# Kernel optimization log

Hardware: AMD Instinct MI355X
Metric: run time of the kernel (lower is better)

The kernel has to match this reference:

```python
import jax, jax.numpy as jnp
import numpy as np
import math

B, S, D = 2, 1024, 1024
H = 16
HD = D // H
E = 8
DFF = 4096
EPS = 1e-5


def _ln(x, g, b):
    m = jnp.mean(x, axis=-1, keepdims=True)
    v = jnp.mean((x - m) ** 2, axis=-1, keepdims=True)
    return (x - m) / jnp.sqrt(v + EPS) * g + b


def setup_inputs() -> dict:
    key = jax.random.key(0)
    ks = jax.random.split(key, 16)
    s = 0.02
    inp = {
        'src': jax.random.normal(ks[0], (B, S, D), jnp.float32),
        'qw': jax.random.normal(ks[1], (D, D), jnp.float32) * s,
        'kw': jax.random.normal(ks[2], (D, D), jnp.float32) * s,
        'vw': jax.random.normal(ks[3], (D, D), jnp.float32) * s,
        'ow': jax.random.normal(ks[4], (D, D), jnp.float32) * s,
        'gate_w': jax.random.normal(ks[5], (D, D), jnp.float32) * s,
        'gate_b': jax.random.normal(ks[6], (D,), jnp.float32) * s,
        'scale_w': jax.random.normal(ks[7], (H, HD), jnp.float32) * s,
        'n1_g': jnp.ones((D,), jnp.float32),
        'n1_b': jnp.zeros((D,), jnp.float32),
        'n2_g': jnp.ones((D,), jnp.float32),
        'n2_b': jnp.zeros((D,), jnp.float32),
        'moe_gate_w': jax.random.normal(ks[8], (D, E), jnp.float32) * s,
        'moe_gate_b': jnp.zeros((E,), jnp.float32),
        'w1': jax.random.normal(ks[9], (E, D, DFF), jnp.float32) * s,
        'b1': jnp.zeros((E, DFF), jnp.float32),
        'ln_g': jnp.ones((E, DFF), jnp.float32),
        'ln_b': jnp.zeros((E, DFF), jnp.float32),
        'w2': jax.random.normal(ks[10], (E, DFF, D), jnp.float32) * s,
        'b2': jnp.zeros((E, D), jnp.float32),
        'res_scale': jnp.ones((E,), jnp.float32),
    }
    return inp


def _forward(src, qw, kw, vw, ow, gate_w, gate_b, scale_w, n1_g, n1_b, n2_g, n2_b,
             moe_gate_w, moe_gate_b, w1, b1, ln_g, ln_b, w2, b2, res_scale):
    # ---- MemoAttention (non-flash path, eval: no dropout, no mask) ----
    q = (src @ qw).reshape(B, S, H, HD).transpose(0, 2, 1, 3)  # [B,H,S,HD]
    k = (src @ kw).reshape(B, S, H, HD).transpose(0, 2, 1, 3)
    v = (src @ vw).reshape(B, S, H, HD).transpose(0, 2, 1, 3)
    scores = jnp.einsum('bhqd,bhkd->bhqk', q, k) / math.sqrt(HD)
    # dynamic per-(head,query) scale gate
    scale = jax.nn.sigmoid(jnp.einsum('bhsd,hd->bhs', q, scale_w)) * 2.0
    scores = scores * scale[..., None]
    attn = jax.nn.softmax(scores, axis=-1)
    out = jnp.einsum('bhqk,bhkd->bhqd', attn, v)
    out = out.transpose(0, 2, 1, 3).reshape(B, S, D)
    gate = jax.nn.sigmoid(out @ gate_w + gate_b)
    attn_out = (out * gate) @ ow

    x = _ln(src + attn_out, n1_g, n1_b)

    # ---- MoE FFN (top-2 routing; eval: no gate noise; capacity never exceeded) ----
    xf = x.reshape(-1, D)                      # [T, D]
    T = xf.shape[0]
    logits = xf @ moe_gate_w + moe_gate_b      # [T, E]
    top_v, top_i = jax.lax.top_k(logits, 2)
    # NB: original sums BOTH top-k softmax weights per token (== 1.0), and the
    wsum = jnp.sum(jax.nn.softmax(top_v, axis=-1), axis=-1)   # [T] (== 1)
    e_sel = jnp.max(top_i, axis=-1)                           # [T]
    # dense per-expert FFN on all tokens, then per-token select (masked compute)
    h = jnp.einsum('td,edf->etf', xf, w1) + b1[:, None, :]    # [E,T,DFF]
    h = _ln(h, ln_g[:, None, :], ln_b[:, None, :])
    h = jax.nn.gelu(h, approximate=False)                     # torch nn.GELU (erf)
    y = jnp.einsum('etf,efd->etd', h, w2) + b2[:, None, :]    # [E,T,D]
    y = y * res_scale[:, None, None] + xf[None]
    sel = jnp.take_along_axis(y, e_sel[None, :, None], axis=0)[0]  # [T,D]
    moe_out = (sel * wsum[:, None]).reshape(B, S, D)

    return _ln(x + moe_out, n2_g, n2_b)


def reference(src, qw, kw, vw, ow, gate_w, gate_b, scale_w, n1_g, n1_b, n2_g, n2_b,
              moe_gate_w, moe_gate_b, w1, b1, ln_g, ln_b, w2, b2, res_scale):
    return _forward(src, qw, kw, vw, ow, gate_w, gate_b, scale_w, n1_g, n1_b,
                    n2_g, n2_b, moe_gate_w, moe_gate_b, w1, b1, ln_g, ln_b,
                    w2, b2, res_scale)
```

## Files before the change

kernel.cpp:

```cpp
#include <hip/hip_runtime.h>
#include <math.h>

#define TOK    2048
#define DMODEL 1024
#define NHEAD  16
#define HDIM   64
#define NEXP   8
#define DFFN   4096

typedef unsigned short u16;
typedef __attribute__((ext_vector_type(8))) short short8;
typedef __attribute__((ext_vector_type(4))) float floatx4;

__device__ __forceinline__ float sigmoidf_(float x) { return 1.f / (1.f + __expf(-x)); }

__device__ __forceinline__ u16 f2bf(float f) {
  union { float f; unsigned u; } v; v.f = f;
  unsigned r = v.u + 0x7FFFu + ((v.u >> 16) & 1u);
  return (u16)(r >> 16);
}
__device__ __forceinline__ float bf2f(u16 h) {
  union { unsigned u; float f; } v; v.u = ((unsigned)h) << 16; return v.f;
}

__device__ __forceinline__ void gload16(const void* g, void* l) {
  __builtin_amdgcn_global_load_lds((const __attribute__((address_space(1))) void*)g,
                                   (__attribute__((address_space(3))) void*)l, 16, 0, 0);
}

__device__ __forceinline__ float blockReduceSum256(float val) {
  __shared__ float ws_[4];
  #pragma unroll
  for (int off = 32; off; off >>= 1) val += __shfl_down(val, off);
  int lane = threadIdx.x & 63, w = threadIdx.x >> 6;
  if (lane == 0) ws_[w] = val;
  __syncthreads();
  float r = ws_[0] + ws_[1] + ws_[2] + ws_[3];
  __syncthreads();
  return r;
}

__global__ __launch_bounds__(256) void prep_kernel(
    const float* __restrict__ src, u16* __restrict__ Shi, u16* __restrict__ Slo,
    const float* __restrict__ Qw, const float* __restrict__ Kw, const float* __restrict__ Vw,
    u16* __restrict__ W3h, u16* __restrict__ W3l,
    const float* __restrict__ Gw, u16* __restrict__ Gh, u16* __restrict__ Gl,
    const float* __restrict__ Ow, u16* __restrict__ Oh, u16* __restrict__ Ol) {
  const int bid = blockIdx.x, tid = threadIdx.x;
  __shared__ float tile[32][33];
  if (bid < 2048) {
    const int i = bid * 256 + tid;
    const float4 v = ((const float4*)src)[i];
    const float f[4] = {v.x, v.y, v.z, v.w};
    union { u16 s[4]; uint2 u; } h, l;
    #pragma unroll
    for (int j = 0; j < 4; ++j) {
      h.s[j] = f2bf(f[j]);
      l.s[j] = f2bf(f[j] - bf2f(h.s[j]));
    }
    ((uint2*)Shi)[i] = h.u;
    ((uint2*)Slo)[i] = l.u;
    return;
  }
  const float* W; u16 *Whp, *Wlp; int n0, k0, ldk;
  if (bid < 5120) {
    const int t = bid - 2048;
    const int z = t >> 5;
    const int zz = z >> 5;
    W = (zz == 0) ? Qw : (zz == 1) ? Kw : Vw;
    Whp = W3h + (size_t)zz * DMODEL * DMODEL;
    Wlp = W3l + (size_t)zz * DMODEL * DMODEL;
    n0 = (t & 31) * 32; k0 = (z & 31) * 32; ldk = DMODEL;
  } else {
    const int t = bid - 5120;
    const int t2 = t & 1023;
    if (t < 1024) { W = Gw; Whp = Gh; Wlp = Gl; }
    else          { W = Ow; Whp = Oh; Wlp = Ol; }
    n0 = (t2 & 31) * 32; k0 = (t2 >> 5) * 32; ldk = DMODEL;
  }
  const int r = tid >> 3, c4 = (tid & 7) * 4;
  const float4 v = *(const float4*)&W[(size_t)(k0 + r) * DMODEL + n0 + c4];
  tile[r][c4+0] = v.x; tile[r][c4+1] = v.y; tile[r][c4+2] = v.z; tile[r][c4+3] = v.w;
  __syncthreads();
  union { u16 s[4]; uint2 u; } h, l;
  #pragma unroll
  for (int j = 0; j < 4; ++j) {
    const float f = tile[c4 + j][r];
    h.s[j] = f2bf(f);
    l.s[j] = f2bf(f - bf2f(h.s[j]));
  }
  *(uint2*)&Whp[(size_t)(n0 + r) * ldk + k0 + c4] = h.u;
  *(uint2*)&Wlp[(size_t)(n0 + r) * ldk + k0 + c4] = l.u;
}

template<int EPI, int TN>
__device__ __forceinline__ void gemm_split_body(
    u16* Ah, u16* Al, u16* Bh, u16* Bl, int bx, int by,
    const u16* __restrict__ Ahi, const u16* __restrict__ Alo,
    const u16* __restrict__ Whi, const u16* __restrict__ Wlo,
    const float* __restrict__ bias, const float* __restrict__ mul,
    float* __restrict__ Cf, u16* __restrict__ Chi, u16* __restrict__ Clo,
    u16* __restrict__ Vth, u16* __restrict__ Vtl,
    int M, int N, int K) {
  constexpr int NF = TN / 32;
  const int tid = threadIdx.x;
  const int lane = tid & 63, wave = tid >> 6;
  const int row0 = by * 128, col0 = bx * TN;
  const int wm = (wave & 1) * 64, wn = (wave >> 1) * (TN / 2);
  const int mr = tid >> 3;
  const int ksrc = (tid & 7) ^ ((tid >> 3) & 7);
  const floatx4 zero = {0.f, 0.f, 0.f, 0.f};
  floatx4 acc[4][NF];
  #pragma unroll
  for (int i = 0; i < 4; ++i)
    #pragma unroll
    for (int j = 0; j < NF; ++j) acc[i][j] = zero;

  for (int k0 = 0; k0 < K; k0 += 64) {
    __syncthreads();
    #pragma unroll
    for (int p = 0; p < 4; ++p) {
      const size_t ga = (size_t)(row0 + p * 32 + mr) * K + (k0 + ksrc * 8);
      const size_t off = (size_t)(p * 256 + wave * 64) * 16;
      gload16(Ahi + ga, (char*)Ah + off);
      gload16(Alo + ga, (char*)Al + off);
    }
    #pragma unroll
    for (int p = 0; p < NF; ++p) {
      const size_t gb = (size_t)(col0 + p * 32 + mr) * K + (k0 + ksrc * 8);
      const size_t off = (size_t)(p * 256 + wave * 64) * 16;
      gload16(Whi + gb, (char*)Bh + off);
      gload16(Wlo + gb, (char*)Bl + off);
    }
    __syncthreads();
    #pragma unroll
    for (int kk = 0; kk < 2; ++kk) {
      short8 ah[4], al[4], bh[NF], bl[NF];
      #pragma unroll
      for (int i = 0; i < 4; ++i) {
        const int ml = wm + i * 16 + (lane & 15);
        const int cm = (kk * 4 + (lane >> 4)) ^ (ml & 7);
        ah[i] = *(const short8*)&Ah[ml * 64 + cm * 8];
        al[i] = *(const short8*)&Al[ml * 64 + cm * 8];
      }
      #pragma unroll
      for (int j = 0; j < NF; ++j) {
        const int nl = wn + j * 16 + (lane & 15);
        const int cn = (kk * 4 + (lane >> 4)) ^ (nl & 7);
        bh[j] = *(const short8*)&Bh[nl * 64 + cn * 8];
        bl[j] = *(const short8*)&Bl[nl * 64 + cn * 8];
      }
      #pragma unroll
      for (int i = 0; i < 4; ++i)
        #pragma unroll
        for (int j = 0; j < NF; ++j) {
          acc[i][j] = __builtin_amdgcn_mfma_f32_16x16x32_bf16(ah[i], bh[j], acc[i][j], 0, 0, 0);
          acc[i][j] = __builtin_amdgcn_mfma_f32_16x16x32_bf16(al[i], bh[j], acc[i][j], 0, 0, 0);
          acc[i][j] = __builtin_amdgcn_mfma_f32_16x16x32_bf16(ah[i], bl[j], acc[i][j], 0, 0, 0);
        }
    }
  }
  const int cl = lane & 15, quad = lane >> 4;
  if (EPI == 2 && col0 >= 2048) {
    #pragma unroll
    for (int i = 0; i < 4; ++i)
      #pragma unroll
      for (int j = 0; j < NF; ++j) {
        const int dg = col0 + wn + j * 16 + cl - 2048;
        const int bh_ = dg >> 6, d = dg & 63;
        const int row = row0 + wm + i * 16 + quad * 4;
        const int b = row >> 10, t0 = row & 1023;
        union { u16 s[4]; uint2 u; } hh, ll;
        #pragma unroll
        for (int r = 0; r < 4; ++r) {
          const float v = acc[i][j][r];
          hh.s[r] = f2bf(v);
          ll.s[r] = f2bf(v - bf2f(hh.s[r]));
        }
        const size_t base = ((size_t)(b * 16 + bh_) * 64 + d) * 1024 + t0;
        *(uint2*)&Vth[base] = hh.u;
        *(uint2*)&Vtl[base] = ll.u;
      }
    return;
  }
  #pragma unroll
  for (int i = 0; i < 4; ++i)
    #pragma unroll
    for (int j = 0; j < NF; ++j) {
      const int col = col0 + wn + j * 16 + cl;
      #pragma unroll
      for (int r = 0; r < 4; ++r) {
        const int row = row0 + wm + i * 16 + quad * 4 + r;
        const float v = acc[i][j][r];
        if (EPI == 0) {
          Cf[(size_t)row * N + col] = v;
        } else if (EPI == 1) {
          const float s = sigmoidf_(v + bias[col]);
          const float g = s * mul[(size_t)row * N + col];
          const u16 hh = f2bf(g);
          Chi[(size_t)row * N + col] = hh;
          Clo[(size_t)row * N + col] = f2bf(g - bf2f(hh));
        } else {
          const u16 hh = f2bf(v);
          Chi[(size_t)row * N + col] = hh;
          Clo[(size_t)row * N + col] = f2bf(v - bf2f(hh));
        }
      }
    }
}

template<int EPI, int TN>
__global__ __launch_bounds__(256, TN == 64 ? 3 : 2) void gemm_split_kernel(
    const u16* __restrict__ Ahi, const u16* __restrict__ Alo,
    const u16* __restrict__ Whi, const u16* __restrict__ Wlo,
    const float* __restrict__ bias, const float* __restrict__ mul,
    float* __restrict__ Cf, u16* __restrict__ Chi, u16* __restrict__ Clo,
    u16* __restrict__ Vth, u16* __restrict__ Vtl,
    int M, int N, int K) {
  __shared__ u16 Ah[128*64], Al[128*64], Bh[TN*64], Bl[TN*64];
  gemm_split_body<EPI, TN>(Ah, Al, Bh, Bl, blockIdx.x, blockIdx.y,
      Ahi, Alo, Whi, Wlo, bias, mul, Cf, Chi, Clo, Vth, Vtl, M, N, K);
}

struct GemmShared { u16 Ah[128*64]; u16 Al[128*64]; u16 Bh[64*64]; u16 Bl[64*64]; };
template<int EPI>
__global__ __launch_bounds__(256, 3) void gemm_split_w2_kernel(
    const u16* __restrict__ Ahi, const u16* __restrict__ Alo,
    const u16* __restrict__ Whi, const u16* __restrict__ Wlo,
    const float* __restrict__ bias, const float* __restrict__ mul,
    float* __restrict__ Cf, u16* __restrict__ Chi, u16* __restrict__ Clo,
    const float* __restrict__ W2, u16* __restrict__ W2b, int khalf) {
  __shared__ union { GemmShared g; float tile[32][33]; } sm;
  const int bid = blockIdx.x;
  if (bid < 256) {
    gemm_split_body<EPI, 64>(sm.g.Ah, sm.g.Al, sm.g.Bh, sm.g.Bl, bid & 15, bid >> 4,
        Ahi, Alo, Whi, Wlo, bias, mul, Cf, Chi, Clo, nullptr, nullptr,
        TOK, DMODEL, DMODEL);
    return;
  }
  const int t = bid - 256;
  const int e = t >> 5, n0 = (t & 31) * 32;
  const float* W = W2 + (size_t)e * DFFN * DMODEL;
  u16* O = W2b + (size_t)e * DMODEL * DFFN;
  const int r = threadIdx.x >> 3, c4 = (threadIdx.x & 7) * 4;
  for (int kt = 0; kt < 64; ++kt) {
    const int k0 = khalf * 2048 + kt * 32;
    __syncthreads();
    const float4 v = *(const float4*)&W[(size_t)(k0 + r) * DMODEL + n0 + c4];
    sm.tile[r][c4+0] = v.x; sm.tile[r][c4+1] = v.y;
    sm.tile[r][c4+2] = v.z; sm.tile[r][c4+3] = v.w;
    __syncthreads();
    union { u16 s[4]; uint2 u; } h4;
    #pragma unroll
    for (int j = 0; j < 4; ++j) h4.s[j] = f2bf(sm.tile[c4 + j][r]);
    *(uint2*)&O[(size_t)(n0 + r) * DFFN + k0 + c4] = h4.u;
  }
}

template<int EPI, int TN>
__global__ __launch_bounds__(256, TN == 64 ? 4 : 3) void gemm_moe_kernel(
    const u16* __restrict__ A, const u16* __restrict__ Wt,
    const float* __restrict__ bias,
    const int* __restrict__ perm, const int* __restrict__ offs,
    const int* __restrict__ counts,
    u16* __restrict__ Hout, float* __restrict__ P0, float* __restrict__ P1,
    int N, int K) {
  constexpr int NF = TN / 32;
  const int z = blockIdx.z;
  const int e = (EPI == 0) ? z : (z & 7);
  const int ks = (EPI == 0) ? 0 : (z >> 3);
  const int ne = counts[e];
  const int tm = blockIdx.y;
  if (tm * 128 >= ne) return;
  const int kbeg = (EPI == 0) ? 0 : ks * (K >> 1);
  const int kend = (EPI == 0) ? K : kbeg + (K >> 1);
  __shared__ u16 As_[128*64], Bs_[TN*64];
  __shared__ int toks[128];
  const int tid = threadIdx.x;
  if (tid < 128) {
    const int idx = tm * 128 + tid;
    toks[tid] = perm[offs[e] + (idx < ne ? idx : 0)];
  }
  __syncthreads();
  const int lane = tid & 63, wave = tid >> 6;
  const int wm = (wave & 1) * 64, wn = (wave >> 1) * (TN / 2);
  const int mr = tid >> 3;
  const int ksrc = (tid & 7) ^ ((tid >> 3) & 7);
  size_t abase[4];
  #pragma unroll
  for (int p = 0; p < 4; ++p) abase[p] = (size_t)toks[p * 32 + mr] * K;
  const u16* We = Wt + (size_t)e * N * K;
  const int col0 = blockIdx.x * TN;
  const floatx4 zero = {0.f, 0.f, 0.f, 0.f};
  floatx4 acc[4][NF];
  #pragma unroll
  for (int i = 0; i < 4; ++i)
    #pragma unroll
    for (int j = 0; j < NF; ++j) acc[i][j] = zero;

  for (int k0 = kbeg; k0 < kend; k0 += 64) {
    __syncthreads();
    #pragma unroll
    for (int p = 0; p < 4; ++p) {
      const size_t off = (size_t)(p * 256 + wave * 64) * 16;
      gload16(A + abase[p] + (k0 + ksrc * 8), (char*)As_ + off);
    }
    #pragma unroll
    for (int p = 0; p < NF; ++p) {
      const size_t off = (size_t)(p * 256 + wave * 64) * 16;
      gload16(We + (size_t)(col0 + p * 32 + mr) * K + (k0 + ksrc * 8), (char*)Bs_ + off);
    }
    __syncthreads();
    #pragma unroll
    for (int kk = 0; kk < 2; ++kk) {
      short8 a[4], b[NF];
      #pragma unroll
      for (int i = 0; i < 4; ++i) {
        const int ml = wm + i * 16 + (lane & 15);
        const int cm = (kk * 4 + (lane >> 4)) ^ (ml & 7);
        a[i] = *(const short8*)&As_[ml * 64 + cm * 8];
      }
      #pragma unroll
      for (int j = 0; j < NF; ++j) {
        const int nl = wn + j * 16 + (lane & 15);
        const int cn = (kk * 4 + (lane >> 4)) ^ (nl & 7);
        b[j] = *(const short8*)&Bs_[nl * 64 + cn * 8];
      }
      #pragma unroll
      for (int i = 0; i < 4; ++i)
        #pragma unroll
        for (int j = 0; j < NF; ++j)
          acc[i][j] = __builtin_amdgcn_mfma_f32_16x16x32_bf16(a[i], b[j], acc[i][j], 0, 0, 0);
    }
  }
  const int cl = lane & 15, quad = lane >> 4;
  float* Pp = (EPI == 1) ? (ks ? P1 : P0) : nullptr;
  #pragma unroll
  for (int i = 0; i < 4; ++i)
    #pragma unroll
    for (int j = 0; j < NF; ++j) {
      const int col = col0 + wn + j * 16 + cl;
      #pragma unroll
      for (int r = 0; r < 4; ++r) {
        const int rl = wm + i * 16 + quad * 4 + r;
        if (tm * 128 + rl < ne) {
          const int tok = toks[rl];
          if (EPI == 0)
            Hout[(size_t)tok * N + col] = f2bf(acc[i][j][r] + bias[(size_t)e * N + col]);
          else
            Pp[(size_t)tok * N + col] = acc[i][j][r];
        }
      }
    }
}

struct AttnShared {
  u16 Kh[64*64], Kl[64*64], Vh[64*64], Vl[64*64];
  u16 Ph[8][16*40], Pl[8][16*40];
};
__global__ __launch_bounds__(512, 2) void attn_w1conv_kernel(
    const u16* __restrict__ QKh, const u16* __restrict__ QKl,
    const u16* __restrict__ Vth, const u16* __restrict__ Vtl,
    const float* __restrict__ scale_w,
    float* __restrict__ AOf, u16* __restrict__ AOh, u16* __restrict__ AOl,
    const float* __restrict__ W1, u16* __restrict__ W1b) {
  __shared__ union { AttnShared a; float tile[64][65]; } sm;
  const int bid = blockIdx.x;
  const int tid = threadIdx.x;
  if (bid >= 256) {
    const int s = bid - 256;
    const int e = s >> 6, n0 = (s & 63) * 64;
    const float* W = W1 + (size_t)e * DMODEL * DFFN;
    u16* O = W1b + (size_t)e * DFFN * DMODEL;
    const int r = tid >> 3, c8 = (tid & 7) * 8;
    for (int k0 = 0; k0 < DMODEL; k0 += 64) {
      __syncthreads();
      const float4 v0 = *(const float4*)&W[(size_t)(k0 + r) * DFFN + n0 + c8];
      const float4 v1 = *(const float4*)&W[(size_t)(k0 + r) * DFFN + n0 + c8 + 4];
      sm.tile[r][c8+0] = v0.x; sm.tile[r][c8+1] = v0.y;
      sm.tile[r][c8+2] = v0.z; sm.tile[r][c8+3] = v0.w;
      sm.tile[r][c8+4] = v1.x; sm.tile[r][c8+5] = v1.y;
      sm.tile[r][c8+6] = v1.z; sm.tile[r][c8+7] = v1.w;
      __syncthreads();
      union { u16 s_[8]; uint4 u; } h8;
      #pragma unroll
      for (int j = 0; j < 8; ++j) h8.s_[j] = f2bf(sm.tile[c8 + j][r]);
      *(uint4*)&O[(size_t)(n0 + r) * DMODEL + k0 + c8] = h8.u;
    }
    return;
  }
  const int qt = bid & 7, h = (bid >> 3) & 15, b = bid >> 7;
  const int lane = tid & 63, wave = tid >> 6;
  const int i15 = lane & 15, quad = lane >> 4;
  const floatx4 zero = {0.f, 0.f, 0.f, 0.f};

  short8 qh[2], ql[2];
  const size_t qrow = ((size_t)b * 1024 + qt * 128 + wave * 16 + i15) * 3072 + h * 64;
  #pragma unroll
  for (int kk = 0; kk < 2; ++kk) {
    qh[kk] = *(const short8*)&QKh[qrow + kk * 32 + quad * 8];
    ql[kk] = *(const short8*)&QKl[qrow + kk * 32 + quad * 8];
  }
  float dot = 0.f;
  #pragma unroll
  for (int kk = 0; kk < 2; ++kk)
    #pragma unroll
    for (int j = 0; j < 8; ++j) {
      const float sw = scale_w[h * 64 + kk * 32 + quad * 8 + j];
      dot += (bf2f((u16)qh[kk][j]) + bf2f((u16)ql[kk][j])) * sw;
    }
  dot += __shfl_xor(dot, 16);
  dot += __shfl_xor(dot, 32);
  const float g = 2.f * sigmoidf_(dot) * 0.125f;
  float stot[4];
  #pragma unroll
  for (int r = 0; r < 4; ++r) stot[r] = __shfl(g, (lane >> 4) * 4 + r);

  float m_r[4], l_r[4];
  floatx4 Of[4];
  #pragma unroll
  for (int r = 0; r < 4; ++r) { m_r[r] = -1e30f; l_r[r] = 0.f; }
  #pragma unroll
  for (int f = 0; f < 4; ++f) Of[f] = zero;
  u16* PhW = sm.a.Ph[wave];
  u16* PlW = sm.a.Pl[wave];

  const int sr = tid >> 3;
  const int sc = ((tid & 7) ^ (sr & 7)) * 8;
  for (int kt = 0; kt < 16; ++kt) {
    __syncthreads();
    {
      const size_t off = (size_t)wave * 1024;
      const size_t kg = ((size_t)b * 1024 + kt * 64 + sr) * 3072 + 1024 + h * 64 + sc;
      gload16(QKh + kg, (char*)sm.a.Kh + off);
      gload16(QKl + kg, (char*)sm.a.Kl + off);
      const size_t vg = ((size_t)(b * 16 + h) * 64 + sr) * 1024 + kt * 64 + sc;
      gload16(Vth + vg, (char*)sm.a.Vh + off);
      gload16(Vtl + vg, (char*)sm.a.Vl + off);
    }
    __syncthreads();
    float pm[4][4];
    #pragma unroll
    for (int jn = 0; jn < 4; ++jn) {
      floatx4 a = zero;
      #pragma unroll
      for (int kk = 0; kk < 2; ++kk) {
        const int n = jn * 16 + i15;
        const int ch = ((kk * 4 + quad) ^ (n & 7)) * 8;
        const short8 bh = *(const short8*)&sm.a.Kh[n * 64 + ch];
        const short8 bl = *(const short8*)&sm.a.Kl[n * 64 + ch];
        a = __builtin_amdgcn_mfma_f32_16x16x32_bf16(qh[kk], bh, a, 0, 0, 0);
        a = __builtin_amdgcn_mfma_f32_16x16x32_bf16(ql[kk], bh, a, 0, 0, 0);
        a = __builtin_amdgcn_mfma_f32_16x16x32_bf16(qh[kk], bl, a, 0, 0, 0);
      }
      #pragma unroll
      for (int r = 0; r < 4; ++r) pm[jn][r] = a[r] * stot[r];
    }
    float alpha[4];
    #pragma unroll
    for (int r = 0; r < 4; ++r) {
      float mx = fmaxf(fmaxf(pm[0][r], pm[1][r]), fmaxf(pm[2][r], pm[3][r]));
      mx = fmaxf(mx, __shfl_xor(mx, 1));
      mx = fmaxf(mx, __shfl_xor(mx, 2));
      mx = fmaxf(mx, __shfl_xor(mx, 4));
      mx = fmaxf(mx, __shfl_xor(mx, 8));
      const float mn = fmaxf(m_r[r], mx);
      alpha[r] = __expf(m_r[r] - mn);
      m_r[r] = mn;
      float rs = 0.f;
      #pragma unroll
      for (int jn = 0; jn < 4; ++jn) { pm[jn][r] = __expf(pm[jn][r] - mn); rs += pm[jn][r]; }
      rs += __shfl_xor(rs, 1);
      rs += __shfl_xor(rs, 2);
      rs += __shfl_xor(rs, 4);
      rs += __shfl_xor(rs, 8);
      l_r[r] = l_r[r] * alpha[r] + rs;
    }
    #pragma unroll
    for (int f = 0; f < 4; ++f)
      #pragma unroll
      for (int r = 0; r < 4; ++r) Of[f][r] *= alpha[r];
    #pragma unroll
    for (int kk = 0; kk < 2; ++kk) {
      #pragma unroll
      for (int jj = 0; jj < 2; ++jj) {
        const int jn = kk * 2 + jj;
        #pragma unroll
        for (int r = 0; r < 4; ++r) {
          const int a = (quad * 4 + r) * 40 + jj * 16 + i15;
          const u16 hh = f2bf(pm[jn][r]);
          PhW[a] = hh;
          PlW[a] = f2bf(pm[jn][r] - bf2f(hh));
        }
      }
      const short8 pah = *(const short8*)&PhW[i15 * 40 + quad * 8];
      const short8 pal = *(const short8*)&PlW[i15 * 40 + quad * 8];
      #pragma unroll
      for (int f = 0; f < 4; ++f) {
        const int d = f * 16 + i15;
        const int ch = ((kk * 4 + quad) ^ (d & 7)) * 8;
        const short8 vbh = *(const short8*)&sm.a.Vh[d * 64 + ch];
        const short8 vbl = *(const short8*)&sm.a.Vl[d * 64 + ch];
        Of[f] = __builtin_amdgcn_mfma_f32_16x16x32_bf16(pah, vbh, Of[f], 0, 0, 0);
        Of[f] = __builtin_amdgcn_mfma_f32_16x16x32_bf16(pal, vbh, Of[f], 0, 0, 0);
        Of[f] = __builtin_amdgcn_mfma_f32_16x16x32_bf16(pah, vbl, Of[f], 0, 0, 0);
      }
    }
  }
  float inv[4];
  #pragma unroll
  for (int r = 0; r < 4; ++r) inv[r] = 1.f / l_r[r];
  #pragma unroll
  for (int f = 0; f < 4; ++f)
    #pragma unroll
    for (int r = 0; r < 4; ++r) {
      const size_t row = (size_t)b * 1024 + qt * 128 + wave * 16 + quad * 4 + r;
      const int col = h * 64 + f * 16 + i15;
      const float val = Of[f][r] * inv[r];
      AOf[row * 1024 + col] = val;
      const u16 hh = f2bf(val);
      AOh[row * 1024 + col] = hh;
      AOl[row * 1024 + col] = f2bf(val - bf2f(hh));
    }
}

__global__ __launch_bounds__(256) void ln_add_router_kernel(
    const float* __restrict__ A, const float* __restrict__ Bp,
    const float* __restrict__ g, const float* __restrict__ beta,
    float* __restrict__ outf, u16* __restrict__ outh,
    const float* __restrict__ gw, const float* __restrict__ gb,
    int* __restrict__ e_sel) {
  __shared__ float xrow[DMODEL];
  int t = blockIdx.x, tid = threadIdx.x;
  const float* a = A + (size_t)t * DMODEL;
  const float* b = Bp + (size_t)t * DMODEL;
  float v[4]; float s = 0.f;
  #pragma unroll
  for (int i = 0; i < 4; ++i) { int d = tid + i*256; v[i] = a[d] + b[d]; s += v[i]; }
  s = blockReduceSum256(s);
  float mean = s * (1.f/1024.f);
  float q = 0.f;
  #pragma unroll
  for (int i = 0; i < 4; ++i) { float df = v[i]-mean; q += df*df; }
  q = blockReduceSum256(q);
  float rstd = rsqrtf(q*(1.f/1024.f) + 1e-5f);
  #pragma unroll
  for (int i = 0; i < 4; ++i) {
    int d = tid + i*256;
    float val = (v[i]-mean)*rstd*g[d] + beta[d];
    outf[(size_t)t*DMODEL + d] = val;
    outh[(size_t)t*DMODEL + d] = f2bf(val);
    xrow[d] = val;
  }
  __syncthreads();
  if (tid < 64) {
    float acc[NEXP] = {};
    for (int d = tid; d < DMODEL; d += 64) {
      float xv = xrow[d];
      const float* gr = gw + (size_t)d * NEXP;
      #pragma unroll
      for (int e = 0; e < NEXP; ++e) acc[e] += xv * gr[e];
    }
    #pragma unroll
    for (int e = 0; e < NEXP; ++e) {
      #pragma unroll
      for (int off = 32; off; off >>= 1) acc[e] += __shfl_down(acc[e], off);
    }
    if (tid == 0) {
      float lg[NEXP];
      #pragma unroll
      for (int e = 0; e < NEXP; ++e) lg[e] = acc[e] + gb[e];
      int i1 = 0;
      for (int e = 1; e < NEXP; ++e) if (lg[e] > lg[i1]) i1 = e;
      int i2 = -1;
      for (int e = 0; e < NEXP; ++e) {
        if (e == i1) continue;
        if (i2 < 0 || lg[e] > lg[i2]) i2 = e;
      }
      e_sel[t] = (i1 > i2) ? i1 : i2;
    }
  }
}

__global__ __launch_bounds__(256) void ln_final_kernel(
    const float* __restrict__ X, const float* __restrict__ P0,
    const float* __restrict__ P1, const float* __restrict__ B2,
    const float* __restrict__ rsv, const int* __restrict__ e_sel,
    const float* __restrict__ g, const float* __restrict__ beta,
    float* __restrict__ out) {
  int t = blockIdx.x, tid = threadIdx.x;
  const int e = e_sel[t];
  const float rse = rsv[e];
  const float* b2e = B2 + (size_t)e * DMODEL;
  const int d0 = tid * 4;
  const size_t base = (size_t)t * DMODEL + d0;
  const float4 xv = *(const float4*)&X[base];
  const float4 p0v = *(const float4*)&P0[base];
  const float4 p1v = *(const float4*)&P1[base];
  const float4 bv = *(const float4*)&b2e[d0];
  float v[4]; float s = 0.f;
  v[0] = 2.f*xv.x + (p0v.x + p1v.x + bv.x) * rse;
  v[1] = 2.f*xv.y + (p0v.y + p1v.y + bv.y) * rse;
  v[2] = 2.f*xv.z + (p0v.z + p1v.z + bv.z) * rse;
  v[3] = 2.f*xv.w + (p0v.w + p1v.w + bv.w) * rse;
  s = v[0] + v[1] + v[2] + v[3];
  s = blockReduceSum256(s);
  float mean = s * (1.f/1024.f);
  float q = 0.f;
  #pragma unroll
  for (int i = 0; i < 4; ++i) { float df = v[i]-mean; q += df*df; }
  q = blockReduceSum256(q);
  float rstd = rsqrtf(q*(1.f/1024.f) + 1e-5f);
  const float4 g4 = *(const float4*)&g[d0];
  const float4 be4 = *(const float4*)&beta[d0];
  float4 o;
  o.x = (v[0]-mean)*rstd*g4.x + be4.x;
  o.y = (v[1]-mean)*rstd*g4.y + be4.y;
  o.z = (v[2]-mean)*rstd*g4.z + be4.z;
  o.w = (v[3]-mean)*rstd*g4.w + be4.w;
  *(float4*)&out[base] = o;
}

__global__ __launch_bounds__(256) void moe_group_kernel(
    const int* __restrict__ e_sel, int* __restrict__ perm,
    int* __restrict__ g_offs, int* __restrict__ g_counts) {
  __shared__ int cnt[NEXP], offs[NEXP], cur[NEXP];
  int tid = threadIdx.x;
  if (tid < NEXP) cnt[tid] = 0;
  __syncthreads();
  for (int t = tid; t < TOK; t += 256) atomicAdd(&cnt[e_sel[t]], 1);
  __syncthreads();
  if (tid == 0) {
    int run = 0;
    for (int e = 0; e < NEXP; ++e) { offs[e] = run; cur[e] = run; run += cnt[e]; }
  }
  __syncthreads();
  if (tid < NEXP) { g_offs[tid] = offs[tid]; g_counts[tid] = cnt[tid]; }
  for (int t = tid; t < TOK; t += 256) {
    int pos = atomicAdd(&cur[e_sel[t]], 1);
    perm[pos] = t;
  }
}

__global__ __launch_bounds__(256) void moe_ln_gelu_kernel(
    u16* __restrict__ H, const float* __restrict__ ln_g,
    const float* __restrict__ ln_b, const int* __restrict__ e_sel) {
  int t = blockIdx.x, tid = threadIdx.x;
  int e = e_sel[t];
  u16* hp = H + (size_t)t * DFFN;
  float v[16]; float s = 0.f;
  #pragma unroll
  for (int i = 0; i < 4; ++i) {
    const int d = i * 1024 + tid * 4;
    union { uint2 u; u16 q[4]; } hv;
    hv.u = *(const uint2*)&hp[d];
    #pragma unroll
    for (int j = 0; j < 4; ++j) { v[i*4+j] = bf2f(hv.q[j]); s += v[i*4+j]; }
  }
  s = blockReduceSum256(s);
  float mean = s * (1.f/4096.f);
  float q = 0.f;
  #pragma unroll
  for (int i = 0; i < 16; ++i) { float df = v[i]-mean; q += df*df; }
  q = blockReduceSum256(q);
  float rstd = rsqrtf(q*(1.f/4096.f) + 1e-5f);
  const float* gg = ln_g + (size_t)e * DFFN;
  const float* bb = ln_b + (size_t)e * DFFN;
  #pragma unroll
  for (int i = 0; i < 4; ++i) {
    const int d = i * 1024 + tid * 4;
    const float4 g4 = *(const float4*)&gg[d];
    const float4 b4 = *(const float4*)&bb[d];
    const float gf[4] = {g4.x, g4.y, g4.z, g4.w};
    const float bf[4] = {b4.x, b4.y, b4.z, b4.w};
    union { uint2 u; u16 q[4]; } ov;
    #pragma unroll
    for (int j = 0; j < 4; ++j) {
      float xx = (v[i*4+j]-mean)*rstd*gf[j] + bf[j];
      ov.q[j] = f2bf(0.5f * xx * (1.f + erff(xx * 0.7071067811865475f)));
    }
    *(uint2*)&hp[d] = ov.u;
  }
}

extern "C" void kernel_launch(void* const* d_in, const int* in_sizes, int n_in,
                              void* d_out, int out_size, void* d_ws, size_t ws_size,
                              hipStream_t stream) {
  (void)in_sizes; (void)n_in; (void)out_size; (void)ws_size;
  const float* src    = (const float*)d_in[0];
  const float* qw     = (const float*)d_in[1];
  const float* kw     = (const float*)d_in[2];
  const float* vw     = (const float*)d_in[3];
  const float* ow     = (const float*)d_in[4];
  const float* gate_w = (const float*)d_in[5];
  const float* gate_b = (const float*)d_in[6];
  const float* scale_w= (const float*)d_in[7];
  const float* n1_g   = (const float*)d_in[8];
  const float* n1_b   = (const float*)d_in[9];
  const float* n2_g   = (const float*)d_in[10];
  const float* n2_b   = (const float*)d_in[11];
  const float* mgw    = (const float*)d_in[12];
  const float* mgb    = (const float*)d_in[13];
  const float* w1     = (const float*)d_in[14];
  const float* b1     = (const float*)d_in[15];
  const float* ln_g   = (const float*)d_in[16];
  const float* ln_b   = (const float*)d_in[17];
  const float* w2     = (const float*)d_in[18];
  const float* b2     = (const float*)d_in[19];
  const float* rs     = (const float*)d_in[20];

  char* ws = (char*)d_ws;
  const size_t MB = 1024 * 1024;
  u16*   src_hi = (u16*)(ws + 0*MB);
  u16*   src_lo = (u16*)(ws + 4*MB);
  u16*   Wt3_hi = (u16*)(ws + 8*MB);
  u16*   Wt3_lo = (u16*)(ws + 14*MB);
  u16*   gw_hi  = (u16*)(ws + 20*MB);
  u16*   gw_lo  = (u16*)(ws + 22*MB);
  u16*   ow_hi  = (u16*)(ws + 24*MB);
  u16*   ow_lo  = (u16*)(ws + 26*MB);
  u16*   W1A    = (u16*)(ws + 28*MB);
  u16*   W2A    = (u16*)(ws + 92*MB);
  u16*   qkv_hi = (u16*)(ws + 156*MB);
  u16*   qkv_lo = (u16*)(ws + 168*MB);
  u16*   Vt_hi  = (u16*)(ws + 180*MB);
  u16*   Vt_lo  = (u16*)(ws + 184*MB);
  float* ao     = (float*)(ws + 188*MB);
  u16*   ao_hi  = (u16*)(ws + 196*MB);
  u16*   ao_lo  = (u16*)(ws + 200*MB);
  u16*   gb_hi  = (u16*)(ws + 204*MB);
  u16*   gb_lo  = (u16*)(ws + 208*MB);
  float* proj   = (float*)(ws + 212*MB);
  float* x      = (float*)(ws + 220*MB);
  u16*   x_hi   = (u16*)(ws + 228*MB);
  u16*   h      = (u16*)(ws + 232*MB);
  float* p0     = (float*)(ws + 248*MB);
  float* p1     = (float*)(ws + 256*MB);
  int*   e_sel  = (int*)(ws + 264*MB);
  int*   perm   = e_sel + TOK;
  int*   offs   = perm + TOK;
  int*   cnts   = offs + NEXP;

  dim3 blk(256);

  prep_kernel<<<7168, blk, 0, stream>>>(src, src_hi, src_lo,
      qw, kw, vw, Wt3_hi, Wt3_lo, gate_w, gw_hi, gw_lo, ow, ow_hi, ow_lo);

  gemm_split_kernel<2,64><<<dim3(48,16), blk, 0, stream>>>(src_hi, src_lo,
      Wt3_hi, Wt3_lo, nullptr, nullptr, nullptr, qkv_hi, qkv_lo, Vt_hi, Vt_lo,
      TOK, 3072, DMODEL);

  attn_w1conv_kernel<<<768, dim3(512), 0, stream>>>(
      qkv_hi, qkv_lo, Vt_hi, Vt_lo, scale_w, ao, ao_hi, ao_lo, w1, W1A);

  gemm_split_w2_kernel<1><<<512, blk, 0, stream>>>(ao_hi, ao_lo, gw_hi, gw_lo,
      gate_b, ao, nullptr, gb_hi, gb_lo, w2, W2A, 0);

  gemm_split_w2_kernel<0><<<512, blk, 0, stream>>>(gb_hi, gb_lo, ow_hi, ow_lo,
      nullptr, nullptr, proj, nullptr, nullptr, w2, W2A, 1);

  ln_add_router_kernel<<<TOK, blk, 0, stream>>>(src, proj, n1_g, n1_b, x, x_hi,
      mgw, mgb, e_sel);

  moe_group_kernel<<<1, blk, 0, stream>>>(e_sel, perm, offs, cnts);

  gemm_moe_kernel<0,128><<<dim3(DFFN/128, 16, 8), blk, 0, stream>>>(
      x_hi, W1A, b1, perm, offs, cnts, h, nullptr, nullptr, DFFN, DMODEL);

  moe_ln_gelu_kernel<<<TOK, blk, 0, stream>>>(h, ln_g, ln_b, e_sel);

  gemm_moe_kernel<1,64><<<dim3(DMODEL/64, 16, 16), blk, 0, stream>>>(
      h, W2A, nullptr, perm, offs, cnts, nullptr, p0, p1, DMODEL, DFFN);

  ln_final_kernel<<<TOK, blk, 0, stream>>>(x, p0, p1, b2, rs, e_sel, n2_g, n2_b,
      (float*)d_out);
}
```

Measured before the change: 740.6 us.

## Move W1 bf16 transpose-conversion from attention kernel into prep kernel

```diff
diff --git a/kernel.cpp b/kernel.cpp
--- a/kernel.cpp
+++ b/kernel.cpp
@@ -45,9 +45,10 @@
     const float* __restrict__ Qw, const float* __restrict__ Kw, const float* __restrict__ Vw,
     u16* __restrict__ W3h, u16* __restrict__ W3l,
     const float* __restrict__ Gw, u16* __restrict__ Gh, u16* __restrict__ Gl,
-    const float* __restrict__ Ow, u16* __restrict__ Oh, u16* __restrict__ Ol) {
+    const float* __restrict__ Ow, u16* __restrict__ Oh, u16* __restrict__ Ol,
+    const float* __restrict__ W1, u16* __restrict__ W1b) {
   const int bid = blockIdx.x, tid = threadIdx.x;
-  __shared__ float tile[32][33];
+  __shared__ float tile[64][65];
   if (bid < 2048) {
     const int i = bid * 256 + tid;
     const float4 v = ((const float4*)src)[i];
@@ -62,35 +63,60 @@
     ((uint2*)Slo)[i] = l.u;
     return;
   }
-  const float* W; u16 *Whp, *Wlp; int n0, k0, ldk;
-  if (bid < 5120) {
-    const int t = bid - 2048;
-    const int z = t >> 5;
-    const int zz = z >> 5;
-    W = (zz == 0) ? Qw : (zz == 1) ? Kw : Vw;
-    Whp = W3h + (size_t)zz * DMODEL * DMODEL;
-    Wlp = W3l + (size_t)zz * DMODEL * DMODEL;
-    n0 = (t & 31) * 32; k0 = (z & 31) * 32; ldk = DMODEL;
-  } else {
-    const int t = bid - 5120;
-    const int t2 = t & 1023;
-    if (t < 1024) { W = Gw; Whp = Gh; Wlp = Gl; }
-    else          { W = Ow; Whp = Oh; Wlp = Ol; }
-    n0 = (t2 & 31) * 32; k0 = (t2 >> 5) * 32; ldk = DMODEL;
-  }
-  const int r = tid >> 3, c4 = (tid & 7) * 4;
-  const float4 v = *(const float4*)&W[(size_t)(k0 + r) * DMODEL + n0 + c4];
-  tile[r][c4+0] = v.x; tile[r][c4+1] = v.y; tile[r][c4+2] = v.z; tile[r][c4+3] = v.w;
+  if (bid < 7168) {
+    const float* W; u16 *Whp, *Wlp; int n0, k0;
+    if (bid < 5120) {
+      const int t = bid - 2048;
+      const int z = t >> 5;
+      const int zz = z >> 5;
+      W = (zz == 0) ? Qw : (zz == 1) ? Kw : Vw;
+      Whp = W3h + (size_t)zz * DMODEL * DMODEL;
+      Wlp = W3l + (size_t)zz * DMODEL * DMODEL;
+      n0 = (t & 31) * 32; k0 = (z & 31) * 32;
+    } else {
+      const int t = bid - 5120;
+      const int t2 = t & 1023;
+      if (t < 1024) { W = Gw; Whp = Gh; Wlp = Gl; }
+      else          { W = Ow; Whp = Oh; Wlp = Ol; }
+      n0 = (t2 & 31) * 32; k0 = (t2 >> 5) * 32;
+    }
+    const int r = tid >> 3, c4 = (tid & 7) * 4;
+    const float4 v = *(const float4*)&W[(size_t)(k0 + r) * DMODEL + n0 + c4];
+    tile[r][c4+0] = v.x; tile[r][c4+1] = v.y; tile[r][c4+2] = v.z; tile[r][c4+3] = v.w;
+    __syncthreads();
+    union { u16 s[4]; uint2 u; } h, l;
+    #pragma unroll
+    for (int j = 0; j < 4; ++j) {
+      const float f = tile[c4 + j][r];
+      h.s[j] = f2bf(f);
+      l.s[j] = f2bf(f - bf2f(h.s[j]));
+    }
+    *(uint2*)&Whp[(size_t)(n0 + r) * DMODEL + k0 + c4] = h.u;
+    *(uint2*)&Wlp[(size_t)(n0 + r) * DMODEL + k0 + c4] = l.u;
+    return;
+  }
+  const int bid2 = bid - 7168;
+  const int e = bid2 >> 10;
+  const int rem = bid2 & 1023;
+  const int n0 = (rem & 63) * 64;
+  const int k0 = (rem >> 6) * 64;
+  const float* W = W1 + (size_t)e * DMODEL * DFFN;
+  u16* O = W1b + (size_t)e * DFFN * DMODEL;
+  const int r = tid >> 2, c16 = (tid & 3) * 16;
+  #pragma unroll
+  for (int jj = 0; jj < 4; ++jj) {
+    const float4 v = *(const float4*)&W[(size_t)(k0 + r) * DFFN + n0 + c16 + jj * 4];
+    tile[r][c16 + jj*4 + 0] = v.x; tile[r][c16 + jj*4 + 1] = v.y;
+    tile[r][c16 + jj*4 + 2] = v.z; tile[r][c16 + jj*4 + 3] = v.w;
+  }
   __syncthreads();
-  union { u16 s[4]; uint2 u; } h, l;
-  #pragma unroll
-  for (int j = 0; j < 4; ++j) {
-    const float f = tile[c4 + j][r];
-    h.s[j] = f2bf(f);
-    l.s[j] = f2bf(f - bf2f(h.s[j]));
-  }
-  *(uint2*)&Whp[(size_t)(n0 + r) * ldk + k0 + c4] = h.u;
-  *(uint2*)&Wlp[(size_t)(n0 + r) * ldk + k0 + c4] = l.u;
+  union { u16 s[8]; uint4 u; } o0, o1;
+  #pragma unroll
+  for (int j = 0; j < 8; ++j) o0.s[j] = f2bf(tile[c16 + j][r]);
+  #pragma unroll
+  for (int j = 0; j < 8; ++j) o1.s[j] = f2bf(tile[c16 + 8 + j][r]);
+  *(uint4*)&O[(size_t)(n0 + r) * DMODEL + k0 + c16]     = o0.u;
+  *(uint4*)&O[(size_t)(n0 + r) * DMODEL + k0 + c16 + 8] = o1.u;
 }
 
 template<int EPI, int TN>
@@ -354,43 +380,15 @@
     }
 }
 
-struct AttnShared {
-  u16 Kh[64*64], Kl[64*64], Vh[64*64], Vl[64*64];
-  u16 Ph[8][16*40], Pl[8][16*40];
-};
-__global__ __launch_bounds__(512, 2) void attn_w1conv_kernel(
+__global__ __launch_bounds__(512, 2) void attn_mfma_kernel(
     const u16* __restrict__ QKh, const u16* __restrict__ QKl,
     const u16* __restrict__ Vth, const u16* __restrict__ Vtl,
     const float* __restrict__ scale_w,
-    float* __restrict__ AOf, u16* __restrict__ AOh, u16* __restrict__ AOl,
-    const float* __restrict__ W1, u16* __restrict__ W1b) {
-  __shared__ union { AttnShared a; float tile[64][65]; } sm;
-  const int bid = blockIdx.x;
-  const int tid = threadIdx.x;
-  if (bid >= 256) {
-    const int s = bid - 256;
-    const int e = s >> 6, n0 = (s & 63) * 64;
-    const float* W = W1 + (size_t)e * DMODEL * DFFN;
-    u16* O = W1b + (size_t)e * DFFN * DMODEL;
-    const int r = tid >> 3, c8 = (tid & 7) * 8;
-    for (int k0 = 0; k0 < DMODEL; k0 += 64) {
-      __syncthreads();
-      const float4 v0 = *(const float4*)&W[(size_t)(k0 + r) * DFFN + n0 + c8];
-      const float4 v1 = *(const float4*)&W[(size_t)(k0 + r) * DFFN + n0 + c8 + 4];
-      sm.tile[r][c8+0] = v0.x; sm.tile[r][c8+1] = v0.y;
-      sm.tile[r][c8+2] = v0.z; sm.tile[r][c8+3] = v0.w;
-      sm.tile[r][c8+4] = v1.x; sm.tile[r][c8+5] = v1.y;
-      sm.tile[r][c8+6] = v1.z; sm.tile[r][c8+7] = v1.w;
-      __syncthreads();
-      union { u16 s_[8]; uint4 u; } h8;
-      #pragma unroll
-      for (int j = 0; j < 8; ++j) h8.s_[j] = f2bf(sm.tile[c8 + j][r]);
-      *(uint4*)&O[(size_t)(n0 + r) * DMODEL + k0 + c8] = h8.u;
-    }
-    return;
-  }
-  const int qt = bid & 7, h = (bid >> 3) & 15, b = bid >> 7;
-  const int lane = tid & 63, wave = tid >> 6;
+    float* __restrict__ AOf, u16* __restrict__ AOh, u16* __restrict__ AOl) {
+  const int qt = blockIdx.x, h = blockIdx.y, b = blockIdx.z;
+  __shared__ u16 Kh[64*64], Kl[64*64], Vh[64*64], Vl[64*64];
+  __shared__ u16 Ph[8][16*40], Pl[8][16*40];
+  const int tid = threadIdx.x, lane = tid & 63, wave = tid >> 6;
   const int i15 = lane & 15, quad = lane >> 4;
   const floatx4 zero = {0.f, 0.f, 0.f, 0.f};
 
@@ -422,8 +420,8 @@
   for (int r = 0; r < 4; ++r) { m_r[r] = -1e30f; l_r[r] = 0.f; }
   #pragma unroll
   for (int f = 0; f < 4; ++f) Of[f] = zero;
-  u16* PhW = sm.a.Ph[wave];
-  u16* PlW = sm.a.Pl[wave];
+  u16* PhW = Ph[wave];
+  u16* PlW = Pl[wave];
 
   const int sr = tid >> 3;
   const int sc = ((tid & 7) ^ (sr & 7)) * 8;
@@ -432,11 +430,11 @@
     {
       const size_t off = (size_t)wave * 1024;
       const size_t kg = ((size_t)b * 1024 + kt * 64 + sr) * 3072 + 1024 + h * 64 + sc;
-      gload16(QKh + kg, (char*)sm.a.Kh + off);
-      gload16(QKl + kg, (char*)sm.a.Kl + off);
+      gload16(QKh + kg, (char*)Kh + off);
+      gload16(QKl + kg, (char*)Kl + off);
       const size_t vg = ((size_t)(b * 16 + h) * 64 + sr) * 1024 + kt * 64 + sc;
-      gload16(Vth + vg, (char*)sm.a.Vh + off);
-      gload16(Vtl + vg, (char*)sm.a.Vl + off);
+      gload16(Vth + vg, (char*)Vh + off);
+      gload16(Vtl + vg, (char*)Vl + off);
     }
     __syncthreads();
     float pm[4][4];
@@ -447,8 +445,8 @@
       for (int kk = 0; kk < 2; ++kk) {
         const int n = jn * 16 + i15;
         const int ch = ((kk * 4 + quad) ^ (n & 7)) * 8;
-        const short8 bh = *(const short8*)&sm.a.Kh[n * 64 + ch];
-        const short8 bl = *(const short8*)&sm.a.Kl[n * 64 + ch];
+        const short8 bh = *(const short8*)&Kh[n * 64 + ch];
+        const short8 bl = *(const short8*)&Kl[n * 64 + ch];
         a = __builtin_amdgcn_mfma_f32_16x16x32_bf16(qh[kk], bh, a, 0, 0, 0);
         a = __builtin_amdgcn_mfma_f32_16x16x32_bf16(ql[kk], bh, a, 0, 0, 0);
         a = __builtin_amdgcn_mfma_f32_16x16x32_bf16(qh[kk], bl, a, 0, 0, 0);
@@ -499,8 +497,8 @@
       for (int f = 0; f < 4; ++f) {
         const int d = f * 16 + i15;
         const int ch = ((kk * 4 + quad) ^ (d & 7)) * 8;
-        const short8 vbh = *(const short8*)&sm.a.Vh[d * 64 + ch];
-        const short8 vbl = *(const short8*)&sm.a.Vl[d * 64 + ch];
+        const short8 vbh = *(const short8*)&Vh[d * 64 + ch];
+        const short8 vbl = *(const short8*)&Vl[d * 64 + ch];
         Of[f] = __builtin_amdgcn_mfma_f32_16x16x32_bf16(pah, vbh, Of[f], 0, 0, 0);
         Of[f] = __builtin_amdgcn_mfma_f32_16x16x32_bf16(pal, vbh, Of[f], 0, 0, 0);
         Of[f] = __builtin_amdgcn_mfma_f32_16x16x32_bf16(pah, vbl, Of[f], 0, 0, 0);
@@ -743,15 +741,16 @@
 
   dim3 blk(256);
 
-  prep_kernel<<<7168, blk, 0, stream>>>(src, src_hi, src_lo,
-      qw, kw, vw, Wt3_hi, Wt3_lo, gate_w, gw_hi, gw_lo, ow, ow_hi, ow_lo);
+  prep_kernel<<<15360, blk, 0, stream>>>(src, src_hi, src_lo,
+      qw, kw, vw, Wt3_hi, Wt3_lo, gate_w, gw_hi, gw_lo, ow, ow_hi, ow_lo,
+      w1, W1A);
 
   gemm_split_kernel<2,64><<<dim3(48,16), blk, 0, stream>>>(src_hi, src_lo,
       Wt3_hi, Wt3_lo, nullptr, nullptr, nullptr, qkv_hi, qkv_lo, Vt_hi, Vt_lo,
       TOK, 3072, DMODEL);
 
-  attn_w1conv_kernel<<<768, dim3(512), 0, stream>>>(
-      qkv_hi, qkv_lo, Vt_hi, Vt_lo, scale_w, ao, ao_hi, ao_lo, w1, W1A);
+  attn_mfma_kernel<<<dim3(8, NHEAD, 2), dim3(512), 0, stream>>>(
+      qkv_hi, qkv_lo, Vt_hi, Vt_lo, scale_w, ao, ao_hi, ao_lo);
 
   gemm_split_w2_kernel<1><<<512, blk, 0, stream>>>(ao_hi, ao_lo, gw_hi, gw_lo,
       gate_b, ao, nullptr, gb_hi, gb_lo, w2, W2A, 0);
```

New measurement: 713.3 us. 3.7% less time.
